# Performance work log

Measured on AMD Instinct MI355X. Metric: run time of the kernel, lower is better.

The kernel has to match this reference:

```python
import jax, jax.numpy as jnp
import numpy as np

NF = 128  # latent_dim / number of filters


def setup_inputs() -> dict:
    key = jax.random.key(0)
    k1, k2, k3, k4 = jax.random.split(key, 4)
    B, H, W, C = 4, 64, 64, 128
    x = jax.random.normal(k1, (B, H, W, C), dtype=jnp.float32)
    y = jax.random.normal(k2, (B, H, W, C), dtype=jnp.float32)
    # 1x1 conv kernels (C_in, C_out) + biases, glorot-ish scale
    scale = 1.0 / np.sqrt(C)
    W1 = jax.random.normal(k3, (C, NF), dtype=jnp.float32) * scale
    W2 = jax.random.normal(k4, (C, NF), dtype=jnp.float32) * scale
    b1 = jnp.zeros((NF,), dtype=jnp.float32)
    b2 = jnp.zeros((NF,), dtype=jnp.float32)
    return {"x": x, "y": y, "W1": W1, "b1": b1, "W2": W2, "b2": b2}


def reference(x, y, W1, b1, W2, b2):
    B, H, Wd, C = x.shape
    hw = H * Wd
    # 1x1 convs == per-pixel matmul
    xq = jnp.einsum('bhwc,cf->bhwf', x, W1) + b1   # conv1(x)
    yk = jnp.einsum('bhwc,cf->bhwf', y, W2) + b2   # conv2(y)
    xq_r = xq.reshape(B, hw, NF)
    yk_r = yk.reshape(B, hw, NF)
    # A_ij = sigmoid(y_i . x_j), full (hw x hw) sigmoid attention
    A = jax.nn.sigmoid(jnp.einsum('bic,bjc->bij', yk_r, xq_r))
    out = jnp.einsum('bij,bjc->bic', A, yk_r).reshape(B, H, Wd, NF)
    # residual add of the *projected* x (matches original: x was overwritten by conv1)
    out = out + xq
    return out
```

## Files before the change

kernel.cpp:

```cpp
#include <hip/hip_runtime.h>
#include <hip/hip_bf16.h>
#include <stdint.h>

typedef float f32x16 __attribute__((ext_vector_type(16)));
typedef float f32x4  __attribute__((ext_vector_type(4)));
typedef short s16x8  __attribute__((ext_vector_type(8)));
typedef unsigned int u32x4 __attribute__((ext_vector_type(4)));

#define HWSZ   4096
#define NBATCH 4
#define LOG2E  1.44269504088896340736f

__device__ __forceinline__ unsigned short f2bf(float f) {
    unsigned u = __builtin_bit_cast(unsigned, f);
    u += 0x7FFFu + ((u >> 16) & 1u);
    return (unsigned short)(u >> 16);
}
__device__ __forceinline__ unsigned cvt_pk_bf16(float lo, float hi) {
    __hip_bfloat162 h = __float22bfloat162_rn(make_float2(lo, hi));
    return *reinterpret_cast<unsigned*>(&h);
}
__device__ __forceinline__ float sigm2(float s) {
    return __builtin_amdgcn_rcpf(1.f + __builtin_amdgcn_exp2f(-s));
}
__device__ __forceinline__ float bf_lo(unsigned u) {
    return __builtin_bit_cast(float, u << 16);
}
__device__ __forceinline__ float bf_hi(unsigned u) {
    return __builtin_bit_cast(float, u & 0xFFFF0000u);
}

__global__ __launch_bounds__(256, 1) void proj_kernel(
    const float* __restrict__ x, const float* __restrict__ y,
    const float* __restrict__ W1, const float* __restrict__ b1,
    const float* __restrict__ W2, const float* __restrict__ b2,
    float* __restrict__ xq_f32,
    unsigned short* __restrict__ xq_bf,
    unsigned short* __restrict__ yk_bf,
    unsigned short* __restrict__ ykT_bf)
{
    __shared__ unsigned short Xlds[64][136];
    __shared__ unsigned short Ylds[64][136];
    __shared__ unsigned short Tlds[128][72];

    const int t    = threadIdx.x;
    const int lane = t & 63;
    const int w    = t >> 6;
    const int l31  = lane & 31;
    const int g    = lane >> 5;
    const int r0   = blockIdx.x * 64;
    const int b    = r0 >> 12;
    const int j0   = r0 & (HWSZ - 1);

    #pragma unroll
    for (int i = 0; i < 8; ++i) {
        int li = t + 256 * i;
        int row = li >> 5, c = (li & 31) * 4;
        float4 vx = *(const float4*)(x + (size_t)(r0 + row) * 128 + c);
        float4 vy = *(const float4*)(y + (size_t)(r0 + row) * 128 + c);
        *(uint2*)&Xlds[row][c] = make_uint2(cvt_pk_bf16(vx.x, vx.y), cvt_pk_bf16(vx.z, vx.w));
        *(uint2*)&Ylds[row][c] = make_uint2(cvt_pk_bf16(vy.x, vy.y), cvt_pk_bf16(vy.z, vy.w));
    }
    __syncthreads();

    const int m  = w >> 1;
    const int fh = w & 1;
    const float* Wm = m ? W2 : W1;
    const float* bm = m ? b2 : b1;
    const unsigned short* A0 = m ? &Ylds[0][0] : &Xlds[0][0];

    f32x16 acc[2][2];
    #pragma unroll
    for (int i = 0; i < 16; ++i) {
        acc[0][0][i] = 0.f; acc[0][1][i] = 0.f;
        acc[1][0][i] = 0.f; acc[1][1][i] = 0.f;
    }

    #pragma unroll
    for (int ks = 0; ks < 8; ++ks) {
        s16x8 bfr[2];
        #pragma unroll
        for (int ft = 0; ft < 2; ++ft) {
            const float* wp = Wm + (size_t)(ks * 16 + g * 8) * 128 + fh * 64 + ft * 32 + l31;
            #pragma unroll
            for (int i = 0; i < 8; ++i)
                bfr[ft][i] = (short)f2bf(wp[(size_t)i * 128]);
        }
        #pragma unroll
        for (int rt = 0; rt < 2; ++rt) {
            s16x8 af = *(const s16x8*)(A0 + (size_t)(rt * 32 + l31) * 136 + ks * 16 + g * 8);
            acc[rt][0] = __builtin_amdgcn_mfma_f32_32x32x16_bf16(af, bfr[0], acc[rt][0], 0, 0, 0);
            acc[rt][1] = __builtin_amdgcn_mfma_f32_32x32x16_bf16(af, bfr[1], acc[rt][1], 0, 0, 0);
        }
    }

    const float bias_v[2] = { bm[fh * 64 + l31], bm[fh * 64 + 32 + l31] };

    if (m == 0) {
        #pragma unroll
        for (int rt = 0; rt < 2; ++rt)
        #pragma unroll
        for (int ft = 0; ft < 2; ++ft) {
            int f = fh * 64 + ft * 32 + l31;
            #pragma unroll
            for (int r = 0; r < 16; ++r) {
                int row = rt * 32 + (r & 3) + 8 * (r >> 2) + 4 * g;
                float v = acc[rt][ft][r] + bias_v[ft];
                size_t o = (size_t)(r0 + row) * 128 + f;
                xq_f32[o] = v;
                xq_bf[o]  = f2bf(v * LOG2E);
            }
        }
    } else {
        #pragma unroll
        for (int rt = 0; rt < 2; ++rt)
        #pragma unroll
        for (int ft = 0; ft < 2; ++ft) {
            int f = fh * 64 + ft * 32 + l31;
            #pragma unroll
            for (int rg = 0; rg < 4; ++rg) {
                float p0 = acc[rt][ft][4 * rg + 0] + bias_v[ft];
                float p1 = acc[rt][ft][4 * rg + 1] + bias_v[ft];
                float p2 = acc[rt][ft][4 * rg + 2] + bias_v[ft];
                float p3 = acc[rt][ft][4 * rg + 3] + bias_v[ft];
                int jb = rt * 32 + 8 * rg + 4 * g;
                *(uint2*)&Tlds[f][jb] = make_uint2(cvt_pk_bf16(p0, p1), cvt_pk_bf16(p2, p3));
                size_t o = (size_t)(r0 + jb) * 128 + f;
                yk_bf[o]       = f2bf(p0);
                yk_bf[o + 128] = f2bf(p1);
                yk_bf[o + 256] = f2bf(p2);
                yk_bf[o + 384] = f2bf(p3);
            }
        }
    }
    __syncthreads();

    {
        int f  = t >> 1;
        int jh = (t & 1) * 32;
        unsigned short* dst = ykT_bf + ((size_t)(b * 128 + f)) * HWSZ + j0 + jh;
        #pragma unroll
        for (int c = 0; c < 4; ++c)
            *(s16x8*)(dst + c * 8) = *(const s16x8*)&Tlds[f][jh + c * 8];
    }
}

#define KT_STR   136
#define VT_STR   72
#define KT_BYTES (64 * KT_STR * 2)
#define VT_BYTES (128 * VT_STR * 2)
#define BUF_BYTES (KT_BYTES + VT_BYTES)

__global__ __launch_bounds__(256, 2) void attn128_kernel(
    const unsigned short* __restrict__ Kbf,
    const unsigned short* __restrict__ Qbf,
    const unsigned short* __restrict__ Vtbf,
    unsigned* __restrict__ outp)
{
    __shared__ __align__(16) char smem[2 * BUF_BYTES];

    const int t    = threadIdx.x;
    const int lane = t & 63;
    const int qt   = t >> 6;
    const int l31  = lane & 31;
    const int g    = lane >> 5;

    const int split  = blockIdx.x >> 7;
    const int r      = blockIdx.x & 127;
    const int b      = r >> 5;
    const int qb     = (r & 31) * 128;
    const int jBegin = split * (HWSZ / 4);
    const int nt     = (HWSZ / 4) / 64;

    s16x8 qfrag[8];
    {
        const unsigned short* qp =
            Qbf + (((size_t)(b * HWSZ + qb + 32 * qt + l31)) << 7) + g * 8;
        #pragma unroll
        for (int fs = 0; fs < 8; ++fs)
            qfrag[fs] = *(const s16x8*)(qp + fs * 16);
    }

    f32x16 acc[4];
    #pragma unroll
    for (int ft = 0; ft < 4; ++ft)
        #pragma unroll
        for (int i = 0; i < 16; ++i) acc[ft][i] = 0.f;

    f32x16 zv;
    #pragma unroll
    for (int i = 0; i < 16; ++i) zv[i] = 0.f;

    const unsigned short* Kbase = Kbf  + (((size_t)b * HWSZ) << 7);
    const unsigned short* Vbase = Vtbf + (((size_t)b) << 7) * HWSZ;

    const unsigned short* kSrc = Kbase + (size_t)(jBegin + (t >> 4)) * 128 + (t & 15) * 8;
    const unsigned short* vSrc = Vbase + (size_t)(t >> 3) * HWSZ + jBegin + (t & 7) * 8;
    const int kDst = (t >> 4) * KT_STR + (t & 15) * 8;
    const int vDst = (t >> 3) * VT_STR + (t & 7) * 8;

    {
        unsigned short* Kl = (unsigned short*)smem;
        unsigned short* Vl = (unsigned short*)(smem + KT_BYTES);
        #pragma unroll
        for (int i = 0; i < 4; ++i)
            *(s16x8*)(Kl + kDst + i * 16 * KT_STR) = *(const s16x8*)(kSrc + (size_t)i * 2048);
        #pragma unroll
        for (int i = 0; i < 4; ++i)
            *(s16x8*)(Vl + vDst + i * 32 * VT_STR) = *(const s16x8*)(vSrc + (size_t)i * 32 * HWSZ);
    }
    __syncthreads();

    int c = 0;
    for (int it = 0; it < nt; ++it) {
        const bool pre = (it + 1 < nt);
        const unsigned short* Kl = (const unsigned short*)(smem + c * BUF_BYTES);
        const unsigned short* Vl = (const unsigned short*)(smem + c * BUF_BYTES + KT_BYTES);

        s16x8 kf0[8], kf1[8];
        {
            const unsigned short* Krow = Kl + (size_t)l31 * KT_STR + g * 8;
            #pragma unroll
            for (int fs = 0; fs < 8; ++fs)
                kf0[fs] = *(const s16x8*)(Krow + fs * 16);
        }
        f32x16 s0a, s0b;
        __builtin_amdgcn_s_setprio(1);
        #pragma unroll
        for (int fs = 0; fs < 4; ++fs) {
            s0a = __builtin_amdgcn_mfma_f32_32x32x16_bf16(kf0[fs],     qfrag[fs],
                      fs == 0 ? zv : s0a, 0, 0, 0);
            s0b = __builtin_amdgcn_mfma_f32_32x32x16_bf16(kf0[fs + 4], qfrag[fs + 4],
                      fs == 0 ? zv : s0b, 0, 0, 0);
        }
        __builtin_amdgcn_s_setprio(0);

        {
            const unsigned short* Krow = Kl + (size_t)(32 + l31) * KT_STR + g * 8;
            #pragma unroll
            for (int fs = 0; fs < 8; ++fs)
                kf1[fs] = *(const s16x8*)(Krow + fs * 16);
        }
        s16x8 kr[4], vr[4];
        if (pre) {
            kSrc += 64 * 128;
            vSrc += 64;
            #pragma unroll
            for (int i = 0; i < 4; ++i)
                kr[i] = *(const s16x8*)(kSrc + (size_t)i * 2048);
            #pragma unroll
            for (int i = 0; i < 4; ++i)
                vr[i] = *(const s16x8*)(vSrc + (size_t)i * 32 * HWSZ);
        }

        f32x16 s1a, s1b;
        unsigned W0[2][4], W1[2][4];
        #pragma unroll
        for (int fs = 0; fs < 4; ++fs) {
            s1a = __builtin_amdgcn_mfma_f32_32x32x16_bf16(kf1[fs],     qfrag[fs],
                      fs == 0 ? zv : s1a, 0, 0, 0);
            s1b = __builtin_amdgcn_mfma_f32_32x32x16_bf16(kf1[fs + 4], qfrag[fs + 4],
                      fs == 0 ? zv : s1b, 0, 0, 0);
            const int rg = fs;
            float p0 = sigm2(s0a[4 * rg + 0] + s0b[4 * rg + 0]);
            float p1 = sigm2(s0a[4 * rg + 1] + s0b[4 * rg + 1]);
            float p2 = sigm2(s0a[4 * rg + 2] + s0b[4 * rg + 2]);
            float p3 = sigm2(s0a[4 * rg + 3] + s0b[4 * rg + 3]);
            W0[0][rg] = cvt_pk_bf16(p0, p1);
            W1[0][rg] = cvt_pk_bf16(p2, p3);
        }

        __builtin_amdgcn_s_setprio(1);
        #pragma unroll
        for (int s2 = 0; s2 < 2; ++s2) {
            unsigned a0 = W0[0][2 * s2], b0 = W0[0][2 * s2 + 1];
            unsigned a1 = W1[0][2 * s2], b1 = W1[0][2 * s2 + 1];
            asm("v_permlane32_swap_b32 %0, %1" : "+v"(a0), "+v"(b0));
            asm("v_permlane32_swap_b32 %0, %1" : "+v"(a1), "+v"(b1));
            u32x4 pw;
            pw[0] = a0; pw[1] = a1; pw[2] = b0; pw[3] = b1;
            s16x8 pf = __builtin_bit_cast(s16x8, pw);
            #pragma unroll
            for (int ft = 0; ft < 4; ++ft) {
                s16x8 vf = *(const s16x8*)(Vl + (size_t)(32 * ft + l31) * VT_STR + s2 * 16 + g * 8);
                acc[ft] = __builtin_amdgcn_mfma_f32_32x32x16_bf16(pf, vf, acc[ft], 0, 0, 0);
            }
            #pragma unroll
            for (int h = 0; h < 2; ++h) {
                const int rg = 2 * s2 + h;
                float p0 = sigm2(s1a[4 * rg + 0] + s1b[4 * rg + 0]);
                float p1 = sigm2(s1a[4 * rg + 1] + s1b[4 * rg + 1]);
                float p2 = sigm2(s1a[4 * rg + 2] + s1b[4 * rg + 2]);
                float p3 = sigm2(s1a[4 * rg + 3] + s1b[4 * rg + 3]);
                W0[1][rg] = cvt_pk_bf16(p0, p1);
                W1[1][rg] = cvt_pk_bf16(p2, p3);
            }
        }

        #pragma unroll
        for (int s2 = 0; s2 < 2; ++s2) {
            unsigned a0 = W0[1][2 * s2], b0 = W0[1][2 * s2 + 1];
            unsigned a1 = W1[1][2 * s2], b1 = W1[1][2 * s2 + 1];
            asm("v_permlane32_swap_b32 %0, %1" : "+v"(a0), "+v"(b0));
            asm("v_permlane32_swap_b32 %0, %1" : "+v"(a1), "+v"(b1));
            u32x4 pw;
            pw[0] = a0; pw[1] = a1; pw[2] = b0; pw[3] = b1;
            s16x8 pf = __builtin_bit_cast(s16x8, pw);
            const int ks = 2 + s2;
            #pragma unroll
            for (int ft = 0; ft < 4; ++ft) {
                s16x8 vf = *(const s16x8*)(Vl + (size_t)(32 * ft + l31) * VT_STR + ks * 16 + g * 8);
                acc[ft] = __builtin_amdgcn_mfma_f32_32x32x16_bf16(pf, vf, acc[ft], 0, 0, 0);
            }
        }
        __builtin_amdgcn_s_setprio(0);

        if (pre) {
            unsigned short* Kd = (unsigned short*)(smem + (c ^ 1) * BUF_BYTES);
            unsigned short* Vd = (unsigned short*)(smem + (c ^ 1) * BUF_BYTES + KT_BYTES);
            #pragma unroll
            for (int i = 0; i < 4; ++i)
                *(s16x8*)(Kd + kDst + i * 16 * KT_STR) = kr[i];
            #pragma unroll
            for (int i = 0; i < 4; ++i)
                *(s16x8*)(Vd + vDst + i * 32 * VT_STR) = vr[i];
        }
        __syncthreads();
        c ^= 1;
    }

    unsigned* op = outp + (size_t)split * ((size_t)NBATCH * HWSZ * 64);
    #pragma unroll
    for (int ft = 0; ft < 4; ++ft)
    #pragma unroll
    for (int pr = 0; pr < 8; ++pr) {
        int r2 = 2 * pr;
        int row = (r2 & 3) + 8 * (r2 >> 2) + 4 * g;
        int q = qb + 32 * qt + row;
        unsigned v = cvt_pk_bf16(acc[ft][r2], acc[ft][r2 + 1]);
        op[((size_t)(b * HWSZ + q) >> 1) * 128 + 32 * ft + l31] = v;
    }
}

template<bool SPLIT>
__global__ __launch_bounds__(256, 2) void attn_kernel(
    const unsigned short* __restrict__ Kbf,
    const unsigned short* __restrict__ Qbf,
    const unsigned short* __restrict__ Vtbf,
    const float* __restrict__ resid,
    float* __restrict__ outp)
{
    __shared__ __align__(16) char smem[2 * BUF_BYTES];

    const int t    = threadIdx.x;
    const int lane = t & 63;
    const int w    = t >> 6;
    const int qt   = w & 1;
    const int jt   = w >> 1;
    const int l31  = lane & 31;
    const int g    = lane >> 5;

    int bid = blockIdx.x;
    int half = 0;
    if (SPLIT) { half = bid >> 8; bid &= 255; }
    const int b      = bid >> 6;
    const int qb     = (bid & 63) * 64;
    const int jBegin = half * (HWSZ / 2);
    const int nt     = (SPLIT ? HWSZ / 2 : HWSZ) / 64;

    s16x8 qfrag[8];
    {
        const unsigned short* qp =
            Qbf + (((size_t)(b * HWSZ + qb + 32 * qt + l31)) << 7) + g * 8;
        #pragma unroll
        for (int fs = 0; fs < 8; ++fs)
            qfrag[fs] = *(const s16x8*)(qp + fs * 16);
    }

    f32x16 acc[4];
    #pragma unroll
    for (int ft = 0; ft < 4; ++ft)
        #pragma unroll
        for (int i = 0; i < 16; ++i) acc[ft][i] = 0.f;

    const unsigned short* Kbase = Kbf  + (((size_t)b * HWSZ) << 7);
    const unsigned short* Vbase = Vtbf + (((size_t)b) << 7) * HWSZ;

    const unsigned short* kSrc = Kbase + (size_t)(jBegin + (t >> 4)) * 128 + (t & 15) * 8;
    const unsigned short* vSrc = Vbase + (size_t)(t >> 3) * HWSZ + jBegin + (t & 7) * 8;
    const int kDst = (t >> 4) * KT_STR + (t & 15) * 8;
    const int vDst = (t >> 3) * VT_STR + (t & 7) * 8;

    {
        unsigned short* Kl = (unsigned short*)smem;
        unsigned short* Vl = (unsigned short*)(smem + KT_BYTES);
        #pragma unroll
        for (int i = 0; i < 4; ++i)
            *(s16x8*)(Kl + kDst + i * 16 * KT_STR) = *(const s16x8*)(kSrc + (size_t)i * 2048);
        #pragma unroll
        for (int i = 0; i < 4; ++i)
            *(s16x8*)(Vl + vDst + i * 32 * VT_STR) = *(const s16x8*)(vSrc + (size_t)i * 32 * HWSZ);
    }
    __syncthreads();

    int c = 0;
    for (int it = 0; it < nt; ++it) {
        const bool pre = (it + 1 < nt);
        s16x8 kr[4], vr[4];
        if (pre) {
            kSrc += 64 * 128;
            vSrc += 64;
            #pragma unroll
            for (int i = 0; i < 4; ++i)
                kr[i] = *(const s16x8*)(kSrc + (size_t)i * 2048);
            #pragma unroll
            for (int i = 0; i < 4; ++i)
                vr[i] = *(const s16x8*)(vSrc + (size_t)i * 32 * HWSZ);
        }

        const unsigned short* Kl = (const unsigned short*)(smem + c * BUF_BYTES);
        const unsigned short* Vl = (const unsigned short*)(smem + c * BUF_BYTES + KT_BYTES);

        f32x16 sa, sb;
        #pragma unroll
        for (int i = 0; i < 16; ++i) { sa[i] = 0.f; sb[i] = 0.f; }
        const unsigned short* Krow = Kl + (size_t)(32 * jt + l31) * KT_STR + g * 8;
        __builtin_amdgcn_s_setprio(1);
        #pragma unroll
        for (int fs = 0; fs < 4; ++fs) {
            sa = __builtin_amdgcn_mfma_f32_32x32x16_bf16(
                     *(const s16x8*)(Krow + fs * 16), qfrag[fs], sa, 0, 0, 0);
            sb = __builtin_amdgcn_mfma_f32_32x32x16_bf16(
                     *(const s16x8*)(Krow + (fs + 4) * 16), qfrag[fs + 4], sb, 0, 0, 0);
        }
        __builtin_amdgcn_s_setprio(0);

        unsigned W0[4], W1[4];
        #pragma unroll
        for (int rg = 0; rg < 4; ++rg) {
            float p0 = sigm2(sa[4 * rg + 0] + sb[4 * rg + 0]);
            float p1 = sigm2(sa[4 * rg + 1] + sb[4 * rg + 1]);
            float p2 = sigm2(sa[4 * rg + 2] + sb[4 * rg + 2]);
            float p3 = sigm2(sa[4 * rg + 3] + sb[4 * rg + 3]);
            W0[rg] = cvt_pk_bf16(p0, p1);
            W1[rg] = cvt_pk_bf16(p2, p3);
        }

        #pragma unroll
        for (int s2 = 0; s2 < 2; ++s2) {
            unsigned a0 = W0[2 * s2], b0 = W0[2 * s2 + 1];
            unsigned a1 = W1[2 * s2], b1 = W1[2 * s2 + 1];
            asm("v_permlane32_swap_b32 %0, %1" : "+v"(a0), "+v"(b0));
            asm("v_permlane32_swap_b32 %0, %1" : "+v"(a1), "+v"(b1));
            u32x4 pw;
            pw[0] = a0; pw[1] = a1; pw[2] = b0; pw[3] = b1;
            s16x8 pf = __builtin_bit_cast(s16x8, pw);
            const int ks = 2 * jt + s2;
            __builtin_amdgcn_s_setprio(1);
            #pragma unroll
            for (int ft = 0; ft < 4; ++ft) {
                s16x8 vf = *(const s16x8*)(Vl + (size_t)(32 * ft + l31) * VT_STR + ks * 16 + g * 8);
                acc[ft] = __builtin_amdgcn_mfma_f32_32x32x16_bf16(pf, vf, acc[ft], 0, 0, 0);
            }
            __builtin_amdgcn_s_setprio(0);
        }

        if (pre) {
            unsigned short* Kd = (unsigned short*)(smem + (c ^ 1) * BUF_BYTES);
            unsigned short* Vd = (unsigned short*)(smem + (c ^ 1) * BUF_BYTES + KT_BYTES);
            #pragma unroll
            for (int i = 0; i < 4; ++i)
                *(s16x8*)(Kd + kDst + i * 16 * KT_STR) = kr[i];
            #pragma unroll
            for (int i = 0; i < 4; ++i)
                *(s16x8*)(Vd + vDst + i * 32 * VT_STR) = vr[i];
        }
        __syncthreads();
        c ^= 1;
    }

    float* red = (float*)smem;
    if (jt == 1) {
        #pragma unroll
        for (int ft = 0; ft < 4; ++ft)
        #pragma unroll
        for (int r = 0; r < 16; ++r) {
            int row = (r & 3) + 8 * (r >> 2) + 4 * g;
            red[qt * 4096 + row * 128 + 32 * ft + l31] = acc[ft][r];
        }
    }
    __syncthreads();
    if (jt == 0) {
        float* op = outp + (SPLIT ? (size_t)half * ((size_t)NBATCH * HWSZ * 128) : 0);
        #pragma unroll
        for (int ft = 0; ft < 4; ++ft)
        #pragma unroll
        for (int r = 0; r < 16; ++r) {
            int row = (r & 3) + 8 * (r >> 2) + 4 * g;
            float v = acc[ft][r] + red[qt * 4096 + row * 128 + 32 * ft + l31];
            int q = qb + 32 * qt + row;
            size_t o = (((size_t)(b * HWSZ + q)) << 7) + 32 * ft + l31;
            if (SPLIT) op[o] = v;
            else       op[o] = v + resid[o];
        }
    }
}

__global__ __launch_bounds__(256, 1) void reduce2_kernel(
    const float* __restrict__ p0, const float* __restrict__ p1, float* outp)
{
    int i = blockIdx.x * 256 + threadIdx.x;
    f32x4 a = ((const f32x4*)p0)[i];
    f32x4 b = ((const f32x4*)p1)[i];
    f32x4 c = ((f32x4*)outp)[i];
    ((f32x4*)outp)[i] = a + b + c;
}

__global__ __launch_bounds__(256, 1) void reduce4bf_kernel(
    const unsigned* __restrict__ parts, float* __restrict__ outp)
{
    const size_t NU = (size_t)NBATCH * HWSZ * 64;
    size_t j0 = ((size_t)blockIdx.x * 256 + threadIdx.x) * 4;
    f32x4 lo, hi;
    #pragma unroll
    for (int e = 0; e < 4; ++e) { lo[e] = 0.f; hi[e] = 0.f; }
    #pragma unroll
    for (int k = 0; k < 4; ++k) {
        u32x4 v = *(const u32x4*)(parts + k * NU + j0);
        #pragma unroll
        for (int e = 0; e < 4; ++e) {
            lo[e] += bf_lo(v[e]);
            hi[e] += bf_hi(v[e]);
        }
    }
    size_t p  = j0 >> 7;
    int    f0 = (int)(j0 & 127);
    size_t o0 = (p * 2) * 128 + f0;
    f32x4 r0 = *(const f32x4*)(outp + o0);
    f32x4 r1 = *(const f32x4*)(outp + o0 + 128);
    *(f32x4*)(outp + o0)       = r0 + lo;
    *(f32x4*)(outp + o0 + 128) = r1 + hi;
}

extern "C" void kernel_launch(void* const* d_in, const int* in_sizes, int n_in,
                              void* d_out, int out_size, void* d_ws, size_t ws_size,
                              hipStream_t stream) {
    const float* x  = (const float*)d_in[0];
    const float* y  = (const float*)d_in[1];
    const float* W1 = (const float*)d_in[2];
    const float* b1 = (const float*)d_in[3];
    const float* W2 = (const float*)d_in[4];
    const float* b2 = (const float*)d_in[5];
    float* out = (float*)d_out;

    const size_t NELEM = (size_t)NBATCH * HWSZ * 128;
    unsigned short* xq_bf  = (unsigned short*)d_ws;
    unsigned short* yk_bf  = xq_bf + NELEM;
    unsigned short* ykT_bf = yk_bf + NELEM;
    float* part = (float*)(ykT_bf + NELEM);

    proj_kernel<<<(int)(NBATCH * HWSZ / 64), 256, 0, stream>>>(
        x, y, W1, b1, W2, b2, out, xq_bf, yk_bf, ykT_bf);

    if (ws_size >= NELEM * (6 + 16)) {
        attn128_kernel<<<512, 256, 0, stream>>>(xq_bf, yk_bf, ykT_bf, (unsigned*)part);
        reduce4bf_kernel<<<(int)(NELEM / 2 / 4 / 256), 256, 0, stream>>>((unsigned*)part, out);
    } else if (ws_size >= NELEM * (6 + 8)) {
        attn_kernel<true><<<512, 256, 0, stream>>>(xq_bf, yk_bf, ykT_bf, out, part);
        reduce2_kernel<<<(int)(NELEM / 1024), 256, 0, stream>>>(part, part + NELEM, out);
    } else {
        attn_kernel<false><<<256, 256, 0, stream>>>(xq_bf, yk_bf, ykT_bf, out, out);
    }
}
```

Before: 63.91 us.

## Halve projection tile and pass residual as bf16 to final reduce

The projection kernel now processes 32 rows per block instead of 64, with smaller LDS arrays and launch bounds allowing two blocks per CU, so twice as many blocks run. In the 4-way split path, the projected x residual is written as bf16 to workspace instead of fp32 into the output. The reduce kernel then reads that bf16 residual and writes the output once, avoiding an fp32 read-modify-write of the output. This adds bf16 rounding error on the residual term and needs a larger workspace layout.

```diff
diff --git a/kernel.cpp b/kernel.cpp
--- a/kernel.cpp
+++ b/kernel.cpp
@@ -29,31 +29,36 @@
 __device__ __forceinline__ float bf_hi(unsigned u) {
     return __builtin_bit_cast(float, u & 0xFFFF0000u);
 }
-
-__global__ __launch_bounds__(256, 1) void proj_kernel(
+__device__ __forceinline__ float bf2f(unsigned short u) {
+    return __builtin_bit_cast(float, (unsigned)u << 16);
+}
+
+template<bool WF32>
+__global__ __launch_bounds__(256, 2) void proj_kernel(
     const float* __restrict__ x, const float* __restrict__ y,
     const float* __restrict__ W1, const float* __restrict__ b1,
     const float* __restrict__ W2, const float* __restrict__ b2,
     float* __restrict__ xq_f32,
+    unsigned short* __restrict__ xqu_bf,
     unsigned short* __restrict__ xq_bf,
     unsigned short* __restrict__ yk_bf,
     unsigned short* __restrict__ ykT_bf)
 {
-    __shared__ unsigned short Xlds[64][136];
-    __shared__ unsigned short Ylds[64][136];
-    __shared__ unsigned short Tlds[128][72];
+    __shared__ unsigned short Xlds[32][136];
+    __shared__ unsigned short Ylds[32][136];
+    __shared__ unsigned short Tlds[128][40];
 
     const int t    = threadIdx.x;
     const int lane = t & 63;
     const int w    = t >> 6;
     const int l31  = lane & 31;
     const int g    = lane >> 5;
-    const int r0   = blockIdx.x * 64;
+    const int r0   = blockIdx.x * 32;
     const int b    = r0 >> 12;
     const int j0   = r0 & (HWSZ - 1);
 
     #pragma unroll
-    for (int i = 0; i < 8; ++i) {
+    for (int i = 0; i < 4; ++i) {
         int li = t + 256 * i;
         int row = li >> 5, c = (li & 31) * 4;
         float4 vx = *(const float4*)(x + (size_t)(r0 + row) * 128 + c);
@@ -69,12 +74,9 @@
     const float* bm = m ? b2 : b1;
     const unsigned short* A0 = m ? &Ylds[0][0] : &Xlds[0][0];
 
-    f32x16 acc[2][2];
-    #pragma unroll
-    for (int i = 0; i < 16; ++i) {
-        acc[0][0][i] = 0.f; acc[0][1][i] = 0.f;
-        acc[1][0][i] = 0.f; acc[1][1][i] = 0.f;
-    }
+    f32x16 acc[2];
+    #pragma unroll
+    for (int i = 0; i < 16; ++i) { acc[0][i] = 0.f; acc[1][i] = 0.f; }
 
     #pragma unroll
     for (int ks = 0; ks < 8; ++ks) {
@@ -86,44 +88,38 @@
             for (int i = 0; i < 8; ++i)
                 bfr[ft][i] = (short)f2bf(wp[(size_t)i * 128]);
         }
-        #pragma unroll
-        for (int rt = 0; rt < 2; ++rt) {
-            s16x8 af = *(const s16x8*)(A0 + (size_t)(rt * 32 + l31) * 136 + ks * 16 + g * 8);
-            acc[rt][0] = __builtin_amdgcn_mfma_f32_32x32x16_bf16(af, bfr[0], acc[rt][0], 0, 0, 0);
-            acc[rt][1] = __builtin_amdgcn_mfma_f32_32x32x16_bf16(af, bfr[1], acc[rt][1], 0, 0, 0);
-        }
+        s16x8 af = *(const s16x8*)(A0 + (size_t)l31 * 136 + ks * 16 + g * 8);
+        acc[0] = __builtin_amdgcn_mfma_f32_32x32x16_bf16(af, bfr[0], acc[0], 0, 0, 0);
+        acc[1] = __builtin_amdgcn_mfma_f32_32x32x16_bf16(af, bfr[1], acc[1], 0, 0, 0);
     }
 
     const float bias_v[2] = { bm[fh * 64 + l31], bm[fh * 64 + 32 + l31] };
 
     if (m == 0) {
-        #pragma unroll
-        for (int rt = 0; rt < 2; ++rt)
         #pragma unroll
         for (int ft = 0; ft < 2; ++ft) {
             int f = fh * 64 + ft * 32 + l31;
             #pragma unroll
             for (int r = 0; r < 16; ++r) {
-                int row = rt * 32 + (r & 3) + 8 * (r >> 2) + 4 * g;
-                float v = acc[rt][ft][r] + bias_v[ft];
+                int row = (r & 3) + 8 * (r >> 2) + 4 * g;
+                float v = acc[ft][r] + bias_v[ft];
                 size_t o = (size_t)(r0 + row) * 128 + f;
-                xq_f32[o] = v;
-                xq_bf[o]  = f2bf(v * LOG2E);
+                if (WF32) xq_f32[o] = v;
+                else      xqu_bf[o] = f2bf(v);
+                xq_bf[o] = f2bf(v * LOG2E);
             }
         }
     } else {
-        #pragma unroll
-        for (int rt = 0; rt < 2; ++rt)
         #pragma unroll
         for (int ft = 0; ft < 2; ++ft) {
             int f = fh * 64 + ft * 32 + l31;
             #pragma unroll
             for (int rg = 0; rg < 4; ++rg) {
-                float p0 = acc[rt][ft][4 * rg + 0] + bias_v[ft];
-                float p1 = acc[rt][ft][4 * rg + 1] + bias_v[ft];
-                float p2 = acc[rt][ft][4 * rg + 2] + bias_v[ft];
-                float p3 = acc[rt][ft][4 * rg + 3] + bias_v[ft];
-                int jb = rt * 32 + 8 * rg + 4 * g;
+                float p0 = acc[ft][4 * rg + 0] + bias_v[ft];
+                float p1 = acc[ft][4 * rg + 1] + bias_v[ft];
+                float p2 = acc[ft][4 * rg + 2] + bias_v[ft];
+                float p3 = acc[ft][4 * rg + 3] + bias_v[ft];
+                int jb = 8 * rg + 4 * g;
                 *(uint2*)&Tlds[f][jb] = make_uint2(cvt_pk_bf16(p0, p1), cvt_pk_bf16(p2, p3));
                 size_t o = (size_t)(r0 + jb) * 128 + f;
                 yk_bf[o]       = f2bf(p0);
@@ -137,10 +133,10 @@
 
     {
         int f  = t >> 1;
-        int jh = (t & 1) * 32;
+        int jh = (t & 1) * 16;
         unsigned short* dst = ykT_bf + ((size_t)(b * 128 + f)) * HWSZ + j0 + jh;
         #pragma unroll
-        for (int c = 0; c < 4; ++c)
+        for (int c = 0; c < 2; ++c)
             *(s16x8*)(dst + c * 8) = *(const s16x8*)&Tlds[f][jh + c * 8];
     }
 }
@@ -517,7 +513,8 @@
 }
 
 __global__ __launch_bounds__(256, 1) void reduce4bf_kernel(
-    const unsigned* __restrict__ parts, float* __restrict__ outp)
+    const unsigned* __restrict__ parts, const unsigned short* __restrict__ xqu,
+    float* __restrict__ outp)
 {
     const size_t NU = (size_t)NBATCH * HWSZ * 64;
     size_t j0 = ((size_t)blockIdx.x * 256 + threadIdx.x) * 4;
@@ -536,10 +533,12 @@
     size_t p  = j0 >> 7;
     int    f0 = (int)(j0 & 127);
     size_t o0 = (p * 2) * 128 + f0;
-    f32x4 r0 = *(const f32x4*)(outp + o0);
-    f32x4 r1 = *(const f32x4*)(outp + o0 + 128);
-    *(f32x4*)(outp + o0)       = r0 + lo;
-    *(f32x4*)(outp + o0 + 128) = r1 + hi;
+    const ushort4 r0 = *(const ushort4*)(xqu + o0);
+    const ushort4 r1 = *(const ushort4*)(xqu + o0 + 128);
+    lo[0] += bf2f(r0.x); lo[1] += bf2f(r0.y); lo[2] += bf2f(r0.z); lo[3] += bf2f(r0.w);
+    hi[0] += bf2f(r1.x); hi[1] += bf2f(r1.y); hi[2] += bf2f(r1.z); hi[3] += bf2f(r1.w);
+    *(f32x4*)(outp + o0)       = lo;
+    *(f32x4*)(outp + o0 + 128) = hi;
 }
 
 extern "C" void kernel_launch(void* const* d_in, const int* in_sizes, int n_in,
@@ -557,18 +556,23 @@
     unsigned short* xq_bf  = (unsigned short*)d_ws;
     unsigned short* yk_bf  = xq_bf + NELEM;
     unsigned short* ykT_bf = yk_bf + NELEM;
+    unsigned short* xqu_bf = ykT_bf + NELEM;
+    unsigned* partu = (unsigned*)(xqu_bf + NELEM);
     float* part = (float*)(ykT_bf + NELEM);
 
-    proj_kernel<<<(int)(NBATCH * HWSZ / 64), 256, 0, stream>>>(
-        x, y, W1, b1, W2, b2, out, xq_bf, yk_bf, ykT_bf);
-
-    if (ws_size >= NELEM * (6 + 16)) {
-        attn128_kernel<<<512, 256, 0, stream>>>(xq_bf, yk_bf, ykT_bf, (unsigned*)part);
-        reduce4bf_kernel<<<(int)(NELEM / 2 / 4 / 256), 256, 0, stream>>>((unsigned*)part, out);
-    } else if (ws_size >= NELEM * (6 + 8)) {
+    if (ws_size >= NELEM * 16) {
+        proj_kernel<false><<<(int)(NBATCH * HWSZ / 32), 256, 0, stream>>>(
+            x, y, W1, b1, W2, b2, nullptr, xqu_bf, xq_bf, yk_bf, ykT_bf);
+        attn128_kernel<<<512, 256, 0, stream>>>(xq_bf, yk_bf, ykT_bf, partu);
+        reduce4bf_kernel<<<(int)(NELEM / 2048), 256, 0, stream>>>(partu, xqu_bf, out);
+    } else if (ws_size >= NELEM * 14) {
+        proj_kernel<true><<<(int)(NBATCH * HWSZ / 32), 256, 0, stream>>>(
+            x, y, W1, b1, W2, b2, out, nullptr, xq_bf, yk_bf, ykT_bf);
         attn_kernel<true><<<512, 256, 0, stream>>>(xq_bf, yk_bf, ykT_bf, out, part);
         reduce2_kernel<<<(int)(NELEM / 1024), 256, 0, stream>>>(part, part + NELEM, out);
     } else {
+        proj_kernel<true><<<(int)(NBATCH * HWSZ / 32), 256, 0, stream>>>(
+            x, y, W1, b1, W2, b2, out, nullptr, xq_bf, yk_bf, ykT_bf);
         attn_kernel<false><<<256, 256, 0, stream>>>(xq_bf, yk_bf, ykT_bf, out, out);
     }
 }
```

Measured after the change: 60.83 us, median of 2. -4.8%, faster.
